# Kernel tuning notes

Measured on AMD Instinct MI355X. Metric: run time of the kernel, lower is better.

The kernel has to match this reference:

```python
import jax, jax.numpy as jnp
import numpy as np

NEG_SLOPE = 0.2  # PyG GATConv default negative_slope


def gat_conv(x, edge_index, W, att_src, att_dst, bias):
    """PyG-style GATConv (concat heads, add_self_loops=True, eval mode).
    x: [N, F_in], edge_index: [2, E] (row 0 = src j, row 1 = dst i).
    W: [F_in, H*C], att_src/att_dst: [H, C], bias: [H*C].
    """
    N = x.shape[0]
    H, C = att_src.shape
    loops = jnp.arange(N, dtype=edge_index.dtype)
    src = jnp.concatenate([edge_index[0], loops])  # [E+N]
    dst = jnp.concatenate([edge_index[1], loops])
    h = (x @ W).reshape(N, H, C)                              # [N,H,C]
    a_src = jnp.einsum('nhc,hc->nh', h, att_src)              # [N,H]
    a_dst = jnp.einsum('nhc,hc->nh', h, att_dst)
    alpha = jax.nn.leaky_relu(a_src[src] + a_dst[dst], NEG_SLOPE)  # [E+N,H]
    # segment softmax over edges sharing the same destination node
    m = jax.ops.segment_max(alpha, dst, num_segments=N)       # [N,H]
    e = jnp.exp(alpha - jax.lax.stop_gradient(m)[dst])
    denom = jax.ops.segment_sum(e, dst, num_segments=N)       # [N,H]
    a = e / (denom[dst] + 1e-16)                              # [E+N,H]
    msg = h[src] * a[:, :, None]                              # [E+N,H,C]
    out = jax.ops.segment_sum(msg, dst, num_segments=N)       # [N,H,C]
    return out.reshape(N, H * C) + bias


def setup_inputs() -> dict:
    key = jax.random.key(0)
    ks = jax.random.split(key, 10)
    N, F, NC, C1, H1 = 50000, 128, 40, 16, 8
    E = 800000
    x = jax.random.normal(ks[0], (N, F), dtype=jnp.float32)
    edge_index = jax.random.randint(ks[1], (2, E), 0, N, dtype=jnp.int64)
    s1 = 1.0 / np.sqrt(F)
    W1 = jax.random.uniform(ks[2], (F, H1 * C1), jnp.float32, -s1, s1)
    att_src1 = jax.random.uniform(ks[3], (H1, C1), jnp.float32, -1.0, 1.0) * s1
    att_dst1 = jax.random.uniform(ks[4], (H1, C1), jnp.float32, -1.0, 1.0) * s1
    bias1 = jnp.zeros((H1 * C1,), jnp.float32)
    s2 = 1.0 / np.sqrt(H1 * C1)
    W2 = jax.random.uniform(ks[5], (H1 * C1, NC), jnp.float32, -s2, s2)
    att_src2 = jax.random.uniform(ks[6], (1, NC), jnp.float32, -1.0, 1.0) * s2
    att_dst2 = jax.random.uniform(ks[7], (1, NC), jnp.float32, -1.0, 1.0) * s2
    bias2 = jnp.zeros((NC,), jnp.float32)
    return {"x": x, "edge_index": edge_index, "W1": W1, "att_src1": att_src1,
            "att_dst1": att_dst1, "bias1": bias1, "W2": W2, "att_src2": att_src2,
            "att_dst2": att_dst2, "bias2": bias2}


def reference(x, edge_index, W1, att_src1, att_dst1, bias1, W2, att_src2, att_dst2, bias2):
    h = gat_conv(x, edge_index, W1, att_src1, att_dst1, bias1)   # [N, 128]
    # dropout in eval mode = identity
    out = gat_conv(h, edge_index, W2, att_src2, att_dst2, bias2)  # [N, 40]
    return out
```

## Files before the change

### kernel.cpp

```cpp
#include <hip/hip_runtime.h>
#include <hip/hip_bf16.h>
#include <math.h>

#define NEG_SLOPE 0.2f
#define WSZ 512

typedef __bf16 bf16x8 __attribute__((ext_vector_type(8)));
typedef float f32x4 __attribute__((ext_vector_type(4)));

__device__ __forceinline__ float lrelu(float x) { return x > 0.f ? x : NEG_SLOPE * x; }

__device__ __forceinline__ unsigned short f2bfu(float f) {
    unsigned int ua = __float_as_uint(f);
    return (unsigned short)((ua + 0x7fffu + ((ua >> 16) & 1u)) >> 16);
}
__device__ __forceinline__ float bfu2f(unsigned short u) {
    return __uint_as_float(((unsigned int)u) << 16);
}
__device__ __forceinline__ float bf_lo(unsigned int u) { return __uint_as_float(u << 16); }
__device__ __forceinline__ float bf_hi(unsigned int u) { return __uint_as_float(u & 0xffff0000u); }

__global__ __launch_bounds__(256) void k_prep(const float* __restrict__ W1,
                                              bf16x8* __restrict__ Wp,
                                              const float* __restrict__ W2,
                                              bf16x8* __restrict__ W2p,
                                              const float* __restrict__ att_s1,
                                              const float* __restrict__ att_d1,
                                              const float* __restrict__ att_s2,
                                              const float* __restrict__ att_d2,
                                              int* __restrict__ cnt, int N) {
    int g = blockIdx.x * 256 + threadIdx.x;
    if (g < 2048) {
        int n = g & 15, quad = (g >> 4) & 3, c = (g >> 6) & 3, ct = g >> 8;
        bf16x8 v;
#pragma unroll
        for (int j = 0; j < 8; ++j)
            v[j] = (__bf16)W1[(c * 32 + quad * 8 + j) * 128 + ct * 16 + n];
        Wp[g] = v;
    } else if (g < 2560) {
        int idx = g - 2048;
        int n = idx & 15, quad = (idx >> 4) & 3, c = (idx >> 6) & 3, t8 = idx >> 8;
        int h = n & 7;
        const float* av = (n < 8) ? att_s1 : att_d1;
        bf16x8 vv;
#pragma unroll
        for (int j = 0; j < 8; ++j) {
            int f = c * 32 + quad * 8 + j;
            float full = 0.f;
            for (int cc = 0; cc < 16; ++cc)
                full += W1[f * 128 + h * 16 + cc] * av[h * 16 + cc];
            __bf16 hi = (__bf16)full;
            vv[j] = t8 ? (__bf16)(full - (float)hi) : hi;
        }
        Wp[g] = vv;
    } else if (g < 3328) {
        int idx = g - 2560;
        int n = idx & 15, quad = (idx >> 4) & 3, c = (idx >> 6) & 3, ct = idx >> 8;
        int colc = ct * 16 + n;
        bf16x8 v;
        if (colc < 40) {
#pragma unroll
            for (int j = 0; j < 8; ++j)
                v[j] = (__bf16)W2[(c * 32 + quad * 8 + j) * 40 + colc];
        } else if (ct == 2 && n >= 8 && n < 12) {
            const float* av = (n & 1) ? att_d2 : att_s2;
#pragma unroll
            for (int j = 0; j < 8; ++j) {
                int f = c * 32 + quad * 8 + j;
                float full = 0.f;
                for (int cc = 0; cc < 40; ++cc) full += W2[f * 40 + cc] * av[cc];
                __bf16 hi = (__bf16)full;
                v[j] = (n >= 10) ? (__bf16)(full - (float)hi) : hi;
            }
        } else {
#pragma unroll
            for (int j = 0; j < 8; ++j) v[j] = (__bf16)0.f;
        }
        W2p[idx] = v;
    }
    if (g < N) cnt[g] = 0;
}

__global__ __launch_bounds__(256) void k_hist(const int* __restrict__ ei, int E, int N,
                                              int* __restrict__ cnt,
                                              unsigned short* __restrict__ rank) {
    int e = blockIdx.x * 256 + threadIdx.x;
    if (e >= E + N) return;
    int d = (e < E) ? ei[E + e] : (e - E);
    rank[e] = (unsigned short)atomicAdd(&cnt[d], 1);
}

__global__ __launch_bounds__(256) void k_scan_part(const int* __restrict__ cnt, int N,
                                                   int* __restrict__ psum) {
    __shared__ int sh[256];
    int t = threadIdx.x;
    int base = blockIdx.x * 1024 + t * 4;
    int tl = 0;
#pragma unroll
    for (int j = 0; j < 4; ++j) tl += (base + j < N) ? cnt[base + j] : 0;
    sh[t] = tl; __syncthreads();
    for (int off = 128; off > 0; off >>= 1) {
        if (t < off) sh[t] += sh[t + off];
        __syncthreads();
    }
    if (t == 0) psum[blockIdx.x] = sh[0];
}

__global__ __launch_bounds__(256) void k_scan_add(const int* __restrict__ cnt, int N,
                                                  const int* __restrict__ psum,
                                                  int* __restrict__ rowptr) {
    __shared__ int sh[256];
    __shared__ int basep;
    int t = threadIdx.x;
    if (t == 0) {
        int s = 0;
        for (int i = 0; i < blockIdx.x; ++i) s += psum[i];
        basep = s;
    }
    int base = blockIdx.x * 1024 + t * 4;
    int c[4]; int tl = 0;
#pragma unroll
    for (int j = 0; j < 4; ++j) { c[j] = (base + j < N) ? cnt[base + j] : 0; tl += c[j]; }
    sh[t] = tl; __syncthreads();
    for (int off = 1; off < 256; off <<= 1) {
        int a = (t >= off) ? sh[t - off] : 0;
        __syncthreads();
        sh[t] += a;
        __syncthreads();
    }
    int run = basep + (sh[t] - tl);
#pragma unroll
    for (int j = 0; j < 4; ++j) {
        if (base + j < N) {
            rowptr[base + j] = run; run += c[j];
            if (base + j == N - 1) rowptr[N] = run;
        }
    }
}

__global__ __launch_bounds__(256) void k_scatter(const int* __restrict__ ei, int E, int N,
                                                 const int* __restrict__ rowptr,
                                                 const unsigned short* __restrict__ rank,
                                                 unsigned short* __restrict__ col) {
    int e = blockIdx.x * 256 + threadIdx.x;
    if (e >= E + N) return;
    int s, d;
    if (e < E) { s = ei[e]; d = ei[E + e]; } else { s = d = e - E; }
    col[rowptr[d] + (int)rank[e]] = (unsigned short)s;
}

__global__ __launch_bounds__(256) void k_gemm1(const float* __restrict__ x,
                                               const bf16x8* __restrict__ Wp,
                                               unsigned short* __restrict__ h1A,
                                               unsigned short* __restrict__ h1B,
                                               float* __restrict__ a_src,
                                               float* __restrict__ a_dst, int N) {
    int t = threadIdx.x;
    int w = t >> 6, lane = t & 63, quad = lane >> 4, n16 = lane & 15;
    int row0 = blockIdx.x * 64 + w * 16;
    int arow = row0 + n16; if (arow >= N) arow = N - 1;
    const float* px = x + (size_t)arow * 128;

    bf16x8 ah[4], al[4];
#pragma unroll
    for (int c = 0; c < 4; ++c) {
        float4 v0 = *(const float4*)&px[c * 32 + quad * 8];
        float4 v1 = *(const float4*)&px[c * 32 + quad * 8 + 4];
        float xf[8] = {v0.x, v0.y, v0.z, v0.w, v1.x, v1.y, v1.z, v1.w};
#pragma unroll
        for (int j = 0; j < 8; ++j) {
            __bf16 hi = (__bf16)xf[j];
            ah[c][j] = hi;
            al[c][j] = (__bf16)(xf[j] - (float)hi);
        }
    }

    f32x4 acc[10];
#pragma unroll
    for (int ct = 0; ct < 10; ++ct) acc[ct] = (f32x4){0.f, 0.f, 0.f, 0.f};

    const uint4* wp4 = (const uint4*)Wp;
#pragma unroll
    for (int ct = 0; ct < 10; ++ct) {
#pragma unroll
        for (int c = 0; c < 4; ++c) {
            union { uint4 u; bf16x8 b; } bu;
            bu.u = wp4[((ct * 4 + c) * 4 + quad) * 16 + n16];
            acc[ct] = __builtin_amdgcn_mfma_f32_16x16x32_bf16(ah[c], bu.b, acc[ct], 0, 0, 0);
            acc[ct] = __builtin_amdgcn_mfma_f32_16x16x32_bf16(al[c], bu.b, acc[ct], 0, 0, 0);
        }
    }

    int nodeb = row0 + quad * 4;
#pragma unroll
    for (int ct = 0; ct < 8; ++ct) {
        unsigned short* hp = (ct < 4) ? h1A : h1B;
        int chl = (ct & 3) * 16 + n16;
#pragma unroll
        for (int reg = 0; reg < 4; ++reg) {
            int node = nodeb + reg;
            if (node < N) hp[(size_t)node * 64 + chl] = f2bfu(acc[ct][reg]);
        }
    }
#pragma unroll
    for (int reg = 0; reg < 4; ++reg) {
        int node = nodeb + reg;
        float av = acc[8][reg] + acc[9][reg];
        if (node < N) {
            if (n16 < 8) a_src[(size_t)node * 8 + n16] = av;
            else         a_dst[(size_t)node * 8 + (n16 - 8)] = av;
        }
    }
}

__global__ __launch_bounds__(256) void k_aggr1(const int* __restrict__ rowptr,
                                               const unsigned short* __restrict__ col,
                                               const float* __restrict__ a_src,
                                               const float* __restrict__ a_dst,
                                               const unsigned int* __restrict__ h1A,
                                               const unsigned int* __restrict__ h1B,
                                               const float* __restrict__ bias1,
                                               unsigned int* __restrict__ out1h,
                                               unsigned int* __restrict__ out1l,
                                               int N, int nag) {
    __shared__ float4 evL[WSZ];
    __shared__ int    colL[WSZ];
    __shared__ int    rpL[9];
    __shared__ float4 adL[8];
    int p = (blockIdx.x >= nag) ? 1 : 0;
    int blk = blockIdx.x - p * nag;
    const uint4* hp4 = (const uint4*)(p ? h1B : h1A);
    int t = threadIdx.x;
    int node0 = blk * 8;
    if (t < 9) {
        int nd = node0 + t; if (nd > N) nd = N;
        rpL[t] = rowptr[nd];
    }
    if (t >= 64 && t < 72) {
        int nd = node0 + (t - 64); if (nd >= N) nd = N - 1;
        adL[t - 64] = *(const float4*)&a_dst[(size_t)nd * 8 + p * 4];
    }
    __syncthreads();
    int w0v = rpL[0], end8 = rpL[8];

    int w = t >> 6, lane = t & 63, half = lane >> 5, u = lane & 31;
    int e4 = u >> 3, v = u & 7, hh = v >> 1;
    int idx8 = w * 2 + half;
    int node = node0 + idx8;
    bool nv = (node < N);
    int beg = rpL[idx8], end = rpL[idx8 + 1];

    float den = 0.f;
    float nm[8];
#pragma unroll
    for (int k = 0; k < 8; ++k) nm[k] = 0.f;

    for (int w0 = w0v; w0 < end8; w0 += WSZ) {
        int wend = w0 + WSZ; if (wend > end8) wend = end8;
        int wsz = wend - w0;
        if (w0 != w0v) __syncthreads();
        for (int s = w0 + t; s < wend; s += 256) {
            int su = (int)col[s];
            int lo2 = 0;
            if (rpL[lo2 + 4] <= s) lo2 += 4;
            if (rpL[lo2 + 2] <= s) lo2 += 2;
            if (rpL[lo2 + 1] <= s) lo2 += 1;
            float4 as4 = *(const float4*)&a_src[(size_t)su * 8 + p * 4];
            float4 ad4 = adL[lo2];
            float4 e;
            e.x = __expf(lrelu(as4.x + ad4.x));
            e.y = __expf(lrelu(as4.y + ad4.y));
            e.z = __expf(lrelu(as4.z + ad4.z));
            e.w = __expf(lrelu(as4.w + ad4.w));
            evL[s - w0] = e;
            colL[s - w0] = su;
        }
        __syncthreads();
        int lbeg = (beg > w0) ? beg : w0;
        int lend = (end < wend) ? end : wend;
        int ldeg = lend - lbeg;
        int ldO = __shfl_xor(ldeg, 32);
        int ldm = (ldeg > ldO) ? ldeg : ldO;
        int ob0 = lbeg - w0;
        const float* evf = (const float*)evL;
        for (int c = 0; c < ldm; c += 32) {
            int ccm = ldeg - c; ccm = (ccm < 32) ? ccm : 32;
            int ng = (ccm + 3) >> 2;
            int gl = ng - 1;
            int g1 = (1 < gl) ? 1 : gl;
            int g2 = (2 < gl) ? 2 : gl;
            int g3 = (3 < gl) ? 3 : gl;
            int ob = ob0 + c;
#define CIDX(i) ({ int _x = ob + (i); _x = (_x < 0) ? 0 : _x; (_x >= wsz) ? (wsz - 1) : _x; })
            uint4 U0 = hp4[colL[CIDX(e4)] * 8 + v];
            uint4 U1 = hp4[colL[CIDX(g1 * 4 + e4)] * 8 + v];
            uint4 U2 = hp4[colL[CIDX(g2 * 4 + e4)] * 8 + v];
            uint4 U3 = hp4[colL[CIDX(g3 * 4 + e4)] * 8 + v];
            int body = ng - 4;
            int g = 0;
#pragma unroll 2
            for (; g < body; ++g) {
                uint4 UN = hp4[colL[CIDX((g + 4) * 4 + e4)] * 8 + v];
                int ii = g * 4 + e4;
                float ev = (c + ii < ldeg) ? evf[CIDX(ii) * 4 + hh] : 0.f;
                den += ev;
                nm[0] = fmaf(ev, bf_lo(U0.x), nm[0]);
                nm[1] = fmaf(ev, bf_hi(U0.x), nm[1]);
                nm[2] = fmaf(ev, bf_lo(U0.y), nm[2]);
                nm[3] = fmaf(ev, bf_hi(U0.y), nm[3]);
                nm[4] = fmaf(ev, bf_lo(U0.z), nm[4]);
                nm[5] = fmaf(ev, bf_hi(U0.z), nm[5]);
                nm[6] = fmaf(ev, bf_lo(U0.w), nm[6]);
                nm[7] = fmaf(ev, bf_hi(U0.w), nm[7]);
                U0 = U1; U1 = U2; U2 = U3; U3 = UN;
            }
            for (; g < ng; ++g) {
                int ii = g * 4 + e4;
                float ev = (c + ii < ldeg) ? evf[CIDX(ii) * 4 + hh] : 0.f;
                den += ev;
                nm[0] = fmaf(ev, bf_lo(U0.x), nm[0]);
                nm[1] = fmaf(ev, bf_hi(U0.x), nm[1]);
                nm[2] = fmaf(ev, bf_lo(U0.y), nm[2]);
                nm[3] = fmaf(ev, bf_hi(U0.y), nm[3]);
                nm[4] = fmaf(ev, bf_lo(U0.z), nm[4]);
                nm[5] = fmaf(ev, bf_hi(U0.z), nm[5]);
                nm[6] = fmaf(ev, bf_lo(U0.w), nm[6]);
                nm[7] = fmaf(ev, bf_hi(U0.w), nm[7]);
                U0 = U1; U1 = U2; U2 = U3;
            }
#undef CIDX
        }
    }
    den += __shfl_xor(den, 8);
    den += __shfl_xor(den, 16);
#pragma unroll
    for (int k = 0; k < 8; ++k) {
        nm[k] += __shfl_xor(nm[k], 8);
        nm[k] += __shfl_xor(nm[k], 16);
    }
    if (nv && e4 == 0) {
        float inv = 1.f / (den + 1e-16f);
        float4 b0 = *(const float4*)&bias1[p * 64 + v * 8];
        float4 b1 = *(const float4*)&bias1[p * 64 + v * 8 + 4];
        float bb[8] = {b0.x, b0.y, b0.z, b0.w, b1.x, b1.y, b1.z, b1.w};
        unsigned int H[4], L[4];
#pragma unroll
        for (int q = 0; q < 4; ++q) {
            float o0 = fmaf(nm[2 * q],     inv, bb[2 * q]);
            float o1 = fmaf(nm[2 * q + 1], inv, bb[2 * q + 1]);
            unsigned short h0 = f2bfu(o0), h1 = f2bfu(o1);
            float l0 = o0 - bfu2f(h0), l1 = o1 - bfu2f(h1);
            H[q] = (unsigned int)h0 | ((unsigned int)h1 << 16);
            L[q] = (unsigned int)f2bfu(l0) | ((unsigned int)f2bfu(l1) << 16);
        }
        size_t idx = (size_t)node * 64 + p * 32 + v * 4;
        *(uint4*)&out1h[idx] = make_uint4(H[0], H[1], H[2], H[3]);
        *(uint4*)&out1l[idx] = make_uint4(L[0], L[1], L[2], L[3]);
    }
}

__global__ __launch_bounds__(256) void k_gemm2(const unsigned int* __restrict__ out1h,
                                               const unsigned int* __restrict__ out1l,
                                               const bf16x8* __restrict__ W2p,
                                               unsigned short* __restrict__ h2s,
                                               float* __restrict__ a_src2,
                                               float* __restrict__ a_dst2, int N) {
    int t = threadIdx.x;
    int w = t >> 6, lane = t & 63, quad = lane >> 4, n16 = lane & 15;
    int row0 = blockIdx.x * 64 + w * 16;
    int arow = row0 + n16; if (arow >= N) arow = N - 1;

    bf16x8 ah[4], al[4];
#pragma unroll
    for (int c = 0; c < 4; ++c) {
        size_t base = (size_t)arow * 64 + (c * 32 + quad * 8) / 2;
        union { uint4 u; bf16x8 b; } hu, lu;
        hu.u = *(const uint4*)&out1h[base];
        lu.u = *(const uint4*)&out1l[base];
        ah[c] = hu.b;
        al[c] = lu.b;
    }

    f32x4 acc[3];
#pragma unroll
    for (int ct = 0; ct < 3; ++ct) acc[ct] = (f32x4){0.f, 0.f, 0.f, 0.f};

    const uint4* wp4 = (const uint4*)W2p;
#pragma unroll
    for (int ct = 0; ct < 3; ++ct) {
#pragma unroll
        for (int c = 0; c < 4; ++c) {
            union { uint4 u; bf16x8 b; } bu;
            bu.u = wp4[((ct * 4 + c) * 4 + quad) * 16 + n16];
            acc[ct] = __builtin_amdgcn_mfma_f32_16x16x32_bf16(ah[c], bu.b, acc[ct], 0, 0, 0);
            acc[ct] = __builtin_amdgcn_mfma_f32_16x16x32_bf16(al[c], bu.b, acc[ct], 0, 0, 0);
        }
    }

    int nodeb = row0 + quad * 4;
#pragma unroll
    for (int reg = 0; reg < 4; ++reg) {
        int node = nodeb + reg;
#pragma unroll
        for (int ct = 0; ct < 3; ++ct) {
            int ch = ct * 16 + n16;
            if (node < N && ch < 40) h2s[(size_t)node * 64 + ch] = f2bfu(acc[ct][reg]);
        }
        float fv = acc[2][reg];
        float fused = fv + __shfl_xor(fv, 2);
        if (node < N) {
            if (n16 == 8) a_src2[node] = fused;
            else if (n16 == 9) a_dst2[node] = fused;
        }
    }
}

__global__ __launch_bounds__(256) void k_aggr2(const int* __restrict__ rowptr,
                                               const unsigned short* __restrict__ col,
                                               const float* __restrict__ a_src2,
                                               const float* __restrict__ a_dst2,
                                               const unsigned int* __restrict__ h2b,
                                               const float* __restrict__ bias2,
                                               float* __restrict__ out, int N) {
    __shared__ float evL[WSZ];
    __shared__ int   colL[WSZ];
    __shared__ int   rpL[9];
    __shared__ float adL[8];
    int t = threadIdx.x;
    int node0 = blockIdx.x * 8;
    if (t < 9) {
        int nd = node0 + t; if (nd > N) nd = N;
        rpL[t] = rowptr[nd];
    }
    if (t >= 64 && t < 72) {
        int nd = node0 + (t - 64); if (nd >= N) nd = N - 1;
        adL[t - 64] = a_dst2[nd];
    }
    __syncthreads();
    int w0v = rpL[0], end8 = rpL[8];

    int w = t >> 6, lane = t & 63, half = lane >> 5, u = lane & 31;
    int e4 = u >> 3, v = u & 7;
    int idx8 = w * 2 + half;
    int node = node0 + idx8;
    bool nv = (node < N);
    int beg = rpL[idx8], end = rpL[idx8 + 1];

    const uint4* h24 = (const uint4*)h2b;
    float den = 0.f;
    float am[8];
#pragma unroll
    for (int k = 0; k < 8; ++k) am[k] = 0.f;

    for (int w0 = w0v; w0 < end8; w0 += WSZ) {
        int wend = w0 + WSZ; if (wend > end8) wend = end8;
        int wsz = wend - w0;
        if (w0 != w0v) __syncthreads();
        for (int s = w0 + t; s < wend; s += 256) {
            int su = (int)col[s];
            int lo2 = 0;
            if (rpL[lo2 + 4] <= s) lo2 += 4;
            if (rpL[lo2 + 2] <= s) lo2 += 2;
            if (rpL[lo2 + 1] <= s) lo2 += 1;
            evL[s - w0] = __expf(lrelu(a_src2[su] + adL[lo2]));
            colL[s - w0] = su;
        }
        __syncthreads();
        int lbeg = (beg > w0) ? beg : w0;
        int lend = (end < wend) ? end : wend;
        int ldeg = lend - lbeg;
        int ldO = __shfl_xor(ldeg, 32);
        int ldm = (ldeg > ldO) ? ldeg : ldO;
        int ob0 = lbeg - w0;
        for (int c = 0; c < ldm; c += 32) {
            int ccm = ldeg - c; ccm = (ccm < 32) ? ccm : 32;
            int ng = (ccm + 3) >> 2;
            int gl = ng - 1;
            int g1 = (1 < gl) ? 1 : gl;
            int g2 = (2 < gl) ? 2 : gl;
            int g3 = (3 < gl) ? 3 : gl;
            int ob = ob0 + c;
#define CIDX(i) ({ int _x = ob + (i); _x = (_x < 0) ? 0 : _x; (_x >= wsz) ? (wsz - 1) : _x; })
            uint4 U0 = h24[colL[CIDX(e4)] * 8 + v];
            uint4 U1 = h24[colL[CIDX(g1 * 4 + e4)] * 8 + v];
            uint4 U2 = h24[colL[CIDX(g2 * 4 + e4)] * 8 + v];
            uint4 U3 = h24[colL[CIDX(g3 * 4 + e4)] * 8 + v];
            int body = ng - 4;
            int g = 0;
#pragma unroll 2
            for (; g < body; ++g) {
                uint4 UN = h24[colL[CIDX((g + 4) * 4 + e4)] * 8 + v];
                int ii = g * 4 + e4;
                float evv = (c + ii < ldeg) ? evL[CIDX(ii)] : 0.f;
                den += evv;
                am[0] = fmaf(evv, bf_lo(U0.x), am[0]);
                am[1] = fmaf(evv, bf_hi(U0.x), am[1]);
                am[2] = fmaf(evv, bf_lo(U0.y), am[2]);
                am[3] = fmaf(evv, bf_hi(U0.y), am[3]);
                am[4] = fmaf(evv, bf_lo(U0.z), am[4]);
                am[5] = fmaf(evv, bf_hi(U0.z), am[5]);
                am[6] = fmaf(evv, bf_lo(U0.w), am[6]);
                am[7] = fmaf(evv, bf_hi(U0.w), am[7]);
                U0 = U1; U1 = U2; U2 = U3; U3 = UN;
            }
            for (; g < ng; ++g) {
                int ii = g * 4 + e4;
                float evv = (c + ii < ldeg) ? evL[CIDX(ii)] : 0.f;
                den += evv;
                am[0] = fmaf(evv, bf_lo(U0.x), am[0]);
                am[1] = fmaf(evv, bf_hi(U0.x), am[1]);
                am[2] = fmaf(evv, bf_lo(U0.y), am[2]);
                am[3] = fmaf(evv, bf_hi(U0.y), am[3]);
                am[4] = fmaf(evv, bf_lo(U0.z), am[4]);
                am[5] = fmaf(evv, bf_hi(U0.z), am[5]);
                am[6] = fmaf(evv, bf_lo(U0.w), am[6]);
                am[7] = fmaf(evv, bf_hi(U0.w), am[7]);
                U0 = U1; U1 = U2; U2 = U3;
            }
#undef CIDX
        }
    }
    den += __shfl_xor(den, 8);
    den += __shfl_xor(den, 16);
#pragma unroll
    for (int k = 0; k < 8; ++k) {
        am[k] += __shfl_xor(am[k], 8);
        am[k] += __shfl_xor(am[k], 16);
    }
    if (nv && e4 == 0 && v < 5) {
        float inv = 1.f / (den + 1e-16f);
        float4 b0 = *(const float4*)&bias2[v * 8];
        float4 b1 = *(const float4*)&bias2[v * 8 + 4];
        float4 o0 = make_float4(fmaf(am[0], inv, b0.x), fmaf(am[1], inv, b0.y),
                                fmaf(am[2], inv, b0.z), fmaf(am[3], inv, b0.w));
        float4 o1 = make_float4(fmaf(am[4], inv, b1.x), fmaf(am[5], inv, b1.y),
                                fmaf(am[6], inv, b1.z), fmaf(am[7], inv, b1.w));
        size_t ob = (size_t)node * 40 + v * 8;
        *(float4*)&out[ob] = o0;
        *(float4*)&out[ob + 4] = o1;
    }
}

extern "C" void kernel_launch(void* const* d_in, const int* in_sizes, int n_in,
                              void* d_out, int out_size, void* d_ws, size_t ws_size,
                              hipStream_t stream) {
    const float* x   = (const float*)d_in[0];
    const int*   ei  = (const int*)d_in[1];
    const float* W1  = (const float*)d_in[2];
    const float* as1 = (const float*)d_in[3];
    const float* ad1 = (const float*)d_in[4];
    const float* b1  = (const float*)d_in[5];
    const float* W2  = (const float*)d_in[6];
    const float* as2 = (const float*)d_in[7];
    const float* ad2 = (const float*)d_in[8];
    const float* b2  = (const float*)d_in[9];

    int N = in_sizes[0] / 128;
    int E = in_sizes[1] / 2;
    int EN = E + N;
    size_t Np = (size_t)((N + 3) & ~3);
    size_t ENp = ((size_t)EN + 3) & ~3;

    float* ws = (float*)d_ws;
    unsigned int* out1h = (unsigned int*)ws; ws += Np * 64;
    unsigned int* out1l = (unsigned int*)ws; ws += Np * 64;
    unsigned int* h1A = (unsigned int*)ws; ws += Np * 32;
    unsigned int* h1Bp = (unsigned int*)ws; ws += Np * 32;
    unsigned int* h2b = (unsigned int*)ws; ws += Np * 32;
    float* a_src1  = ws; ws += Np * 8;
    float* a_dst1  = ws; ws += Np * 8;
    float* a_src2v = ws; ws += Np;
    float* a_dst2v = ws; ws += Np;
    bf16x8* Wp  = (bf16x8*)ws; ws += 2560 * 4;
    bf16x8* W2p = (bf16x8*)ws; ws += 768 * 4;
    int* cnt    = (int*)ws; ws += Np;
    int* rowptr = (int*)ws; ws += Np + 4;
    int* psum   = (int*)ws; ws += 256;
    unsigned short* col  = (unsigned short*)ws; ws += ENp / 2 + 4;
    unsigned short* rank = (unsigned short*)ws; ws += ENp / 2 + 4;

    int nb = (N + 1023) / 1024;
    int npre = (N > 3328 ? N : 3328);

    k_prep<<<(npre + 255) / 256, 256, 0, stream>>>(W1, Wp, W2, W2p,
                                                   as1, ad1, as2, ad2, cnt, N);
    k_gemm1<<<(N + 63) / 64, 256, 0, stream>>>(x, Wp,
                                               (unsigned short*)h1A, (unsigned short*)h1Bp,
                                               a_src1, a_dst1, N);
    k_hist<<<(EN + 255) / 256, 256, 0, stream>>>(ei, E, N, cnt, rank);
    k_scan_part<<<nb, 256, 0, stream>>>(cnt, N, psum);
    k_scan_add<<<nb, 256, 0, stream>>>(cnt, N, psum, rowptr);
    k_scatter<<<(EN + 255) / 256, 256, 0, stream>>>(ei, E, N, rowptr, rank, col);

    int nag = (N + 7) / 8;
    k_aggr1<<<2 * nag, 256, 0, stream>>>(rowptr, col, a_src1, a_dst1,
                                         h1A, h1Bp, b1, out1h, out1l, N, nag);
    k_gemm2<<<(N + 63) / 64, 256, 0, stream>>>(out1h, out1l, W2p,
                                               (unsigned short*)h2b, a_src2v, a_dst2v, N);
    k_aggr2<<<nag, 256, 0, stream>>>(rowptr, col, a_src2v, a_dst2v, h2b, b2, (float*)d_out, N);
}
```

Baseline: 235.8 us.

## Merge head-halves in layer-1 aggregation, scatter CSR via atomic cursor, pad edge windows

The layer-1 aggregation kernel now processes both head halves in one block instead of launching two blocks per node group. Edge scores, the col window and a_src are loaded once and reused for both halves. The CSR build drops the per-edge rank array: scatter takes slots with an atomicAdd on a copy of rowptr. Edge windows get zero padding so the clamp arithmetic on LDS indices can be removed. The costs are half as many aggr1 blocks with more registers and LDS each (lower parallelism), more atomic contention in scatter, and a neighbour order that is no longer deterministic.

```diff
diff --git a/kernel.cpp b/kernel.cpp
--- a/kernel.cpp
+++ b/kernel.cpp
@@ -3,7 +3,8 @@
 #include <math.h>
 
 #define NEG_SLOPE 0.2f
-#define WSZ 512
+#define WSZ 384
+#define GZ  32
 
 typedef __bf16 bf16x8 __attribute__((ext_vector_type(8)));
 typedef float f32x4 __attribute__((ext_vector_type(4)));
@@ -82,12 +83,11 @@
 }
 
 __global__ __launch_bounds__(256) void k_hist(const int* __restrict__ ei, int E, int N,
-                                              int* __restrict__ cnt,
-                                              unsigned short* __restrict__ rank) {
+                                              int* __restrict__ cnt) {
     int e = blockIdx.x * 256 + threadIdx.x;
     if (e >= E + N) return;
     int d = (e < E) ? ei[E + e] : (e - E);
-    rank[e] = (unsigned short)atomicAdd(&cnt[d], 1);
+    atomicAdd(&cnt[d], 1);
 }
 
 __global__ __launch_bounds__(256) void k_scan_part(const int* __restrict__ cnt, int N,
@@ -108,7 +108,8 @@
 
 __global__ __launch_bounds__(256) void k_scan_add(const int* __restrict__ cnt, int N,
                                                   const int* __restrict__ psum,
-                                                  int* __restrict__ rowptr) {
+                                                  int* __restrict__ rowptr,
+                                                  int* __restrict__ rp2) {
     __shared__ int sh[256];
     __shared__ int basep;
     int t = threadIdx.x;
@@ -132,21 +133,23 @@
 #pragma unroll
     for (int j = 0; j < 4; ++j) {
         if (base + j < N) {
-            rowptr[base + j] = run; run += c[j];
+            rowptr[base + j] = run;
+            rp2[base + j] = run;
+            run += c[j];
             if (base + j == N - 1) rowptr[N] = run;
         }
     }
 }
 
 __global__ __launch_bounds__(256) void k_scatter(const int* __restrict__ ei, int E, int N,
-                                                 const int* __restrict__ rowptr,
-                                                 const unsigned short* __restrict__ rank,
+                                                 int* __restrict__ rp2,
                                                  unsigned short* __restrict__ col) {
     int e = blockIdx.x * 256 + threadIdx.x;
     if (e >= E + N) return;
     int s, d;
     if (e < E) { s = ei[e]; d = ei[E + e]; } else { s = d = e - E; }
-    col[rowptr[d] + (int)rank[e]] = (unsigned short)s;
+    int slot = atomicAdd(&rp2[d], 1);
+    col[slot] = (unsigned short)s;
 }
 
 __global__ __launch_bounds__(256) void k_gemm1(const float* __restrict__ x,
@@ -222,23 +225,22 @@
                                                const float* __restrict__ bias1,
                                                unsigned int* __restrict__ out1h,
                                                unsigned int* __restrict__ out1l,
-                                               int N, int nag) {
-    __shared__ float4 evL[WSZ];
-    __shared__ int    colL[WSZ];
+                                               int N) {
+    __shared__ float4 evLA[WSZ + GZ];
+    __shared__ float4 evLB[WSZ + GZ];
+    __shared__ int    colL[WSZ + GZ];
     __shared__ int    rpL[9];
-    __shared__ float4 adL[8];
-    int p = (blockIdx.x >= nag) ? 1 : 0;
-    int blk = blockIdx.x - p * nag;
-    const uint4* hp4 = (const uint4*)(p ? h1B : h1A);
+    __shared__ float4 adL[2][8];
     int t = threadIdx.x;
-    int node0 = blk * 8;
+    int node0 = blockIdx.x * 8;
     if (t < 9) {
         int nd = node0 + t; if (nd > N) nd = N;
         rpL[t] = rowptr[nd];
     }
-    if (t >= 64 && t < 72) {
-        int nd = node0 + (t - 64); if (nd >= N) nd = N - 1;
-        adL[t - 64] = *(const float4*)&a_dst[(size_t)nd * 8 + p * 4];
+    if (t >= 64 && t < 80) {
+        int q = t - 64; int pp = q >> 3; int nd = node0 + (q & 7);
+        if (nd >= N) nd = N - 1;
+        adL[pp][q & 7] = *(const float4*)&a_dst[(size_t)nd * 8 + pp * 4];
     }
     __syncthreads();
     int w0v = rpL[0], end8 = rpL[8];
@@ -250,10 +252,12 @@
     bool nv = (node < N);
     int beg = rpL[idx8], end = rpL[idx8 + 1];
 
-    float den = 0.f;
-    float nm[8];
-#pragma unroll
-    for (int k = 0; k < 8; ++k) nm[k] = 0.f;
+    float den[2] = {0.f, 0.f};
+    float nm[2][8];
+#pragma unroll
+    for (int p = 0; p < 2; ++p)
+#pragma unroll
+        for (int k = 0; k < 8; ++k) nm[p][k] = 0.f;
 
     for (int w0 = w0v; w0 < end8; w0 += WSZ) {
         int wend = w0 + WSZ; if (wend > end8) wend = end8;
@@ -265,15 +269,27 @@
             if (rpL[lo2 + 4] <= s) lo2 += 4;
             if (rpL[lo2 + 2] <= s) lo2 += 2;
             if (rpL[lo2 + 1] <= s) lo2 += 1;
-            float4 as4 = *(const float4*)&a_src[(size_t)su * 8 + p * 4];
-            float4 ad4 = adL[lo2];
-            float4 e;
-            e.x = __expf(lrelu(as4.x + ad4.x));
-            e.y = __expf(lrelu(as4.y + ad4.y));
-            e.z = __expf(lrelu(as4.z + ad4.z));
-            e.w = __expf(lrelu(as4.w + ad4.w));
-            evL[s - w0] = e;
+            float4 asA = *(const float4*)&a_src[(size_t)su * 8];
+            float4 asB = *(const float4*)&a_src[(size_t)su * 8 + 4];
+            float4 adA = adL[0][lo2], adB = adL[1][lo2];
+            float4 eA, eB;
+            eA.x = __expf(lrelu(asA.x + adA.x));
+            eA.y = __expf(lrelu(asA.y + adA.y));
+            eA.z = __expf(lrelu(asA.z + adA.z));
+            eA.w = __expf(lrelu(asA.w + adA.w));
+            eB.x = __expf(lrelu(asB.x + adB.x));
+            eB.y = __expf(lrelu(asB.y + adB.y));
+            eB.z = __expf(lrelu(asB.z + adB.z));
+            eB.w = __expf(lrelu(asB.w + adB.w));
+            evLA[s - w0] = eA;
+            evLB[s - w0] = eB;
             colL[s - w0] = su;
+        }
+        if (t < GZ) {
+            float4 z = make_float4(0.f, 0.f, 0.f, 0.f);
+            colL[wsz + t] = 0;
+            evLA[wsz + t] = z;
+            evLB[wsz + t] = z;
         }
         __syncthreads();
         int lbeg = (beg > w0) ? beg : w0;
@@ -282,80 +298,87 @@
         int ldO = __shfl_xor(ldeg, 32);
         int ldm = (ldeg > ldO) ? ldeg : ldO;
         int ob0 = lbeg - w0;
-        const float* evf = (const float*)evL;
-        for (int c = 0; c < ldm; c += 32) {
-            int ccm = ldeg - c; ccm = (ccm < 32) ? ccm : 32;
-            int ng = (ccm + 3) >> 2;
-            int gl = ng - 1;
-            int g1 = (1 < gl) ? 1 : gl;
-            int g2 = (2 < gl) ? 2 : gl;
-            int g3 = (3 < gl) ? 3 : gl;
-            int ob = ob0 + c;
-#define CIDX(i) ({ int _x = ob + (i); _x = (_x < 0) ? 0 : _x; (_x >= wsz) ? (wsz - 1) : _x; })
-            uint4 U0 = hp4[colL[CIDX(e4)] * 8 + v];
-            uint4 U1 = hp4[colL[CIDX(g1 * 4 + e4)] * 8 + v];
-            uint4 U2 = hp4[colL[CIDX(g2 * 4 + e4)] * 8 + v];
-            uint4 U3 = hp4[colL[CIDX(g3 * 4 + e4)] * 8 + v];
-            int body = ng - 4;
-            int g = 0;
+#pragma unroll
+        for (int p = 0; p < 2; ++p) {
+            const uint4* hp4 = (const uint4*)(p ? h1B : h1A);
+            const float* evf = (const float*)(p ? evLB : evLA);
+            for (int c = 0; c < ldm; c += 32) {
+                int ccm = ldeg - c;
+                if (ccm <= 0) continue;
+                if (ccm > 32) ccm = 32;
+                int ng = (ccm + 3) >> 2;
+                int ob = ob0 + c;
+                uint4 U0 = hp4[colL[ob + e4] * 8 + v];
+                uint4 U1 = hp4[colL[ob + 4 + e4] * 8 + v];
+                uint4 U2 = hp4[colL[ob + 8 + e4] * 8 + v];
+                uint4 U3 = hp4[colL[ob + 12 + e4] * 8 + v];
+                int body = ng - 4;
+                int g = 0;
 #pragma unroll 2
-            for (; g < body; ++g) {
-                uint4 UN = hp4[colL[CIDX((g + 4) * 4 + e4)] * 8 + v];
-                int ii = g * 4 + e4;
-                float ev = (c + ii < ldeg) ? evf[CIDX(ii) * 4 + hh] : 0.f;
-                den += ev;
-                nm[0] = fmaf(ev, bf_lo(U0.x), nm[0]);
-                nm[1] = fmaf(ev, bf_hi(U0.x), nm[1]);
-                nm[2] = fmaf(ev, bf_lo(U0.y), nm[2]);
-                nm[3] = fmaf(ev, bf_hi(U0.y), nm[3]);
-                nm[4] = fmaf(ev, bf_lo(U0.z), nm[4]);
-                nm[5] = fmaf(ev, bf_hi(U0.z), nm[5]);
-                nm[6] = fmaf(ev, bf_lo(U0.w), nm[6]);
-                nm[7] = fmaf(ev, bf_hi(U0.w), nm[7]);
-                U0 = U1; U1 = U2; U2 = U3; U3 = UN;
+                for (; g < body; ++g) {
+                    uint4 UN = hp4[colL[ob + (g + 4) * 4 + e4] * 8 + v];
+                    int ii = g * 4 + e4;
+                    float ev = (c + ii < ldeg) ? evf[(ob + ii) * 4 + hh] : 0.f;
+                    den[p] += ev;
+                    nm[p][0] = fmaf(ev, bf_lo(U0.x), nm[p][0]);
+                    nm[p][1] = fmaf(ev, bf_hi(U0.x), nm[p][1]);
+                    nm[p][2] = fmaf(ev, bf_lo(U0.y), nm[p][2]);
+                    nm[p][3] = fmaf(ev, bf_hi(U0.y), nm[p][3]);
+                    nm[p][4] = fmaf(ev, bf_lo(U0.z), nm[p][4]);
+                    nm[p][5] = fmaf(ev, bf_hi(U0.z), nm[p][5]);
+                    nm[p][6] = fmaf(ev, bf_lo(U0.w), nm[p][6]);
+                    nm[p][7] = fmaf(ev, bf_hi(U0.w), nm[p][7]);
+                    U0 = U1; U1 = U2; U2 = U3; U3 = UN;
+                }
+                for (; g < ng; ++g) {
+                    int ii = g * 4 + e4;
+                    float ev = (c + ii < ldeg) ? evf[(ob + ii) * 4 + hh] : 0.f;
+                    den[p] += ev;
+                    nm[p][0] = fmaf(ev, bf_lo(U0.x), nm[p][0]);
+                    nm[p][1] = fmaf(ev, bf_hi(U0.x), nm[p][1]);
+                    nm[p][2] = fmaf(ev, bf_lo(U0.y), nm[p][2]);
+                    nm[p][3] = fmaf(ev, bf_hi(U0.y), nm[p][3]);
+                    nm[p][4] = fmaf(ev, bf_lo(U0.z), nm[p][4]);
+                    nm[p][5] = fmaf(ev, bf_hi(U0.z), nm[p][5]);
+                    nm[p][6] = fmaf(ev, bf_lo(U0.w), nm[p][6]);
+                    nm[p][7] = fmaf(ev, bf_hi(U0.w), nm[p][7]);
+                    U0 = U1; U1 = U2; U2 = U3;
+                }
             }
-            for (; g < ng; ++g) {
-                int ii = g * 4 + e4;
-                float ev = (c + ii < ldeg) ? evf[CIDX(ii) * 4 + hh] : 0.f;
-                den += ev;
-                nm[0] = fmaf(ev, bf_lo(U0.x), nm[0]);
-                nm[1] = fmaf(ev, bf_hi(U0.x), nm[1]);
-                nm[2] = fmaf(ev, bf_lo(U0.y), nm[2]);
-                nm[3] = fmaf(ev, bf_hi(U0.y), nm[3]);
-                nm[4] = fmaf(ev, bf_lo(U0.z), nm[4]);
-                nm[5] = fmaf(ev, bf_hi(U0.z), nm[5]);
-                nm[6] = fmaf(ev, bf_lo(U0.w), nm[6]);
-                nm[7] = fmaf(ev, bf_hi(U0.w), nm[7]);
-                U0 = U1; U1 = U2; U2 = U3;
+        }
+    }
+#pragma unroll
+    for (int p = 0; p < 2; ++p) {
+        float dd = den[p];
+        dd += __shfl_xor(dd, 8);
+        dd += __shfl_xor(dd, 16);
+        float nmv[8];
+#pragma unroll
+        for (int k = 0; k < 8; ++k) {
+            float xv = nm[p][k];
+            xv += __shfl_xor(xv, 8);
+            xv += __shfl_xor(xv, 16);
+            nmv[k] = xv;
+        }
+        if (nv && e4 == 0) {
+            float inv = 1.f / (dd + 1e-16f);
+            float4 b0 = *(const float4*)&bias1[p * 64 + v * 8];
+            float4 b1 = *(const float4*)&bias1[p * 64 + v * 8 + 4];
+            float bb[8] = {b0.x, b0.y, b0.z, b0.w, b1.x, b1.y, b1.z, b1.w};
+            unsigned int H[4], L[4];
+#pragma unroll
+            for (int q = 0; q < 4; ++q) {
+                float o0 = fmaf(nmv[2 * q],     inv, bb[2 * q]);
+                float o1 = fmaf(nmv[2 * q + 1], inv, bb[2 * q + 1]);
+                unsigned short h0 = f2bfu(o0), h1 = f2bfu(o1);
+                float l0 = o0 - bfu2f(h0), l1 = o1 - bfu2f(h1);
+                H[q] = (unsigned int)h0 | ((unsigned int)h1 << 16);
+                L[q] = (unsigned int)f2bfu(l0) | ((unsigned int)f2bfu(l1) << 16);
             }
-#undef CIDX
-        }
-    }
-    den += __shfl_xor(den, 8);
-    den += __shfl_xor(den, 16);
-#pragma unroll
-    for (int k = 0; k < 8; ++k) {
-        nm[k] += __shfl_xor(nm[k], 8);
-        nm[k] += __shfl_xor(nm[k], 16);
-    }
-    if (nv && e4 == 0) {
-        float inv = 1.f / (den + 1e-16f);
-        float4 b0 = *(const float4*)&bias1[p * 64 + v * 8];
-        float4 b1 = *(const float4*)&bias1[p * 64 + v * 8 + 4];
-        float bb[8] = {b0.x, b0.y, b0.z, b0.w, b1.x, b1.y, b1.z, b1.w};
-        unsigned int H[4], L[4];
-#pragma unroll
-        for (int q = 0; q < 4; ++q) {
-            float o0 = fmaf(nm[2 * q],     inv, bb[2 * q]);
-            float o1 = fmaf(nm[2 * q + 1], inv, bb[2 * q + 1]);
-            unsigned short h0 = f2bfu(o0), h1 = f2bfu(o1);
-            float l0 = o0 - bfu2f(h0), l1 = o1 - bfu2f(h1);
-            H[q] = (unsigned int)h0 | ((unsigned int)h1 << 16);
-            L[q] = (unsigned int)f2bfu(l0) | ((unsigned int)f2bfu(l1) << 16);
-        }
-        size_t idx = (size_t)node * 64 + p * 32 + v * 4;
-        *(uint4*)&out1h[idx] = make_uint4(H[0], H[1], H[2], H[3]);
-        *(uint4*)&out1l[idx] = make_uint4(L[0], L[1], L[2], L[3]);
+            size_t idx = (size_t)node * 64 + p * 32 + v * 4;
+            *(uint4*)&out1h[idx] = make_uint4(H[0], H[1], H[2], H[3]);
+            *(uint4*)&out1l[idx] = make_uint4(L[0], L[1], L[2], L[3]);
+        }
     }
 }
 
@@ -422,8 +445,8 @@
                                                const unsigned int* __restrict__ h2b,
                                                const float* __restrict__ bias2,
                                                float* __restrict__ out, int N) {
-    __shared__ float evL[WSZ];
-    __shared__ int   colL[WSZ];
+    __shared__ float evL[WSZ + GZ];
+    __shared__ int   colL[WSZ + GZ];
     __shared__ int   rpL[9];
     __shared__ float adL[8];
     int t = threadIdx.x;
@@ -465,6 +488,10 @@
             evL[s - w0] = __expf(lrelu(a_src2[su] + adL[lo2]));
             colL[s - w0] = su;
         }
+        if (t < GZ) {
+            colL[wsz + t] = 0;
+            evL[wsz + t] = 0.f;
+        }
         __syncthreads();
         int lbeg = (beg > w0) ? beg : w0;
         int lend = (end < wend) ? end : wend;
@@ -473,25 +500,22 @@
         int ldm = (ldeg > ldO) ? ldeg : ldO;
         int ob0 = lbeg - w0;
         for (int c = 0; c < ldm; c += 32) {
-            int ccm = ldeg - c; ccm = (ccm < 32) ? ccm : 32;
+            int ccm = ldeg - c;
+            if (ccm <= 0) continue;
+            if (ccm > 32) ccm = 32;
             int ng = (ccm + 3) >> 2;
-            int gl = ng - 1;
-            int g1 = (1 < gl) ? 1 : gl;
-            int g2 = (2 < gl) ? 2 : gl;
-            int g3 = (3 < gl) ? 3 : gl;
             int ob = ob0 + c;
-#define CIDX(i) ({ int _x = ob + (i); _x = (_x < 0) ? 0 : _x; (_x >= wsz) ? (wsz - 1) : _x; })
-            uint4 U0 = h24[colL[CIDX(e4)] * 8 + v];
-            uint4 U1 = h24[colL[CIDX(g1 * 4 + e4)] * 8 + v];
-            uint4 U2 = h24[colL[CIDX(g2 * 4 + e4)] * 8 + v];
-            uint4 U3 = h24[colL[CIDX(g3 * 4 + e4)] * 8 + v];
+            uint4 U0 = h24[colL[ob + e4] * 8 + v];
+            uint4 U1 = h24[colL[ob + 4 + e4] * 8 + v];
+            uint4 U2 = h24[colL[ob + 8 + e4] * 8 + v];
+            uint4 U3 = h24[colL[ob + 12 + e4] * 8 + v];
             int body = ng - 4;
             int g = 0;
 #pragma unroll 2
             for (; g < body; ++g) {
-                uint4 UN = h24[colL[CIDX((g + 4) * 4 + e4)] * 8 + v];
+                uint4 UN = h24[colL[ob + (g + 4) * 4 + e4] * 8 + v];
                 int ii = g * 4 + e4;
-                float evv = (c + ii < ldeg) ? evL[CIDX(ii)] : 0.f;
+                float evv = (c + ii < ldeg) ? evL[ob + ii] : 0.f;
                 den += evv;
                 am[0] = fmaf(evv, bf_lo(U0.x), am[0]);
                 am[1] = fmaf(evv, bf_hi(U0.x), am[1]);
@@ -505,7 +529,7 @@
             }
             for (; g < ng; ++g) {
                 int ii = g * 4 + e4;
-                float evv = (c + ii < ldeg) ? evL[CIDX(ii)] : 0.f;
+                float evv = (c + ii < ldeg) ? evL[ob + ii] : 0.f;
                 den += evv;
                 am[0] = fmaf(evv, bf_lo(U0.x), am[0]);
                 am[1] = fmaf(evv, bf_hi(U0.x), am[1]);
@@ -517,7 +541,6 @@
                 am[7] = fmaf(evv, bf_hi(U0.w), am[7]);
                 U0 = U1; U1 = U2; U2 = U3;
             }
-#undef CIDX
         }
     }
     den += __shfl_xor(den, 8);
@@ -575,9 +598,9 @@
     bf16x8* W2p = (bf16x8*)ws; ws += 768 * 4;
     int* cnt    = (int*)ws; ws += Np;
     int* rowptr = (int*)ws; ws += Np + 4;
+    int* rp2    = (int*)ws; ws += Np;
     int* psum   = (int*)ws; ws += 256;
     unsigned short* col  = (unsigned short*)ws; ws += ENp / 2 + 4;
-    unsigned short* rank = (unsigned short*)ws; ws += ENp / 2 + 4;
 
     int nb = (N + 1023) / 1024;
     int npre = (N > 3328 ? N : 3328);
@@ -587,14 +610,14 @@
     k_gemm1<<<(N + 63) / 64, 256, 0, stream>>>(x, Wp,
                                                (unsigned short*)h1A, (unsigned short*)h1Bp,
                                                a_src1, a_dst1, N);
-    k_hist<<<(EN + 255) / 256, 256, 0, stream>>>(ei, E, N, cnt, rank);
+    k_hist<<<(EN + 255) / 256, 256, 0, stream>>>(ei, E, N, cnt);
     k_scan_part<<<nb, 256, 0, stream>>>(cnt, N, psum);
-    k_scan_add<<<nb, 256, 0, stream>>>(cnt, N, psum, rowptr);
-    k_scatter<<<(EN + 255) / 256, 256, 0, stream>>>(ei, E, N, rowptr, rank, col);
+    k_scan_add<<<nb, 256, 0, stream>>>(cnt, N, psum, rowptr, rp2);
+    k_scatter<<<(EN + 255) / 256, 256, 0, stream>>>(ei, E, N, rp2, col);
 
     int nag = (N + 7) / 8;
-    k_aggr1<<<2 * nag, 256, 0, stream>>>(rowptr, col, a_src1, a_dst1,
-                                         h1A, h1Bp, b1, out1h, out1l, N, nag);
+    k_aggr1<<<nag, 256, 0, stream>>>(rowptr, col, a_src1, a_dst1,
+                                     h1A, h1Bp, b1, out1h, out1l, N);
     k_gemm2<<<(N + 63) / 64, 256, 0, stream>>>(out1h, out1l, W2p,
                                                (unsigned short*)h2b, a_src2v, a_dst2v, N);
     k_aggr2<<<nag, 256, 0, stream>>>(rowptr, col, a_src2v, a_dst2v, h2b, b2, (float*)d_out, N);
```

New measurement: 263.0 us. 1.12x slower.
